# Kernel optimization log

Hardware: AMD Instinct MI355X
Metric: run time of the kernel (lower is better)

Reference implementation:

```python
import jax, jax.numpy as jnp
import numpy as np

N = 50000      # nodes
E = 800000     # edges (before self-loops)
D = 128        # hid_d
H = 8          # heads
C = D // H     # per-head channels
L = 3          # layers
SLOPE = 0.2    # GATv2 leaky_relu negative slope
EPS = 1e-5     # LayerNorm eps


def setup_inputs() -> dict:
    key = jax.random.key(0)
    ks = jax.random.split(key, 8)
    x = jax.random.normal(ks[0], (N, D), dtype=jnp.float32)
    ei = jax.random.randint(ks[1], (2, E), 0, N, dtype=jnp.int32)
    s = 1.0 / np.sqrt(D)
    Wl = jax.random.normal(ks[2], (L, D, D), dtype=jnp.float32) * s   # source transform per layer
    Wr = jax.random.normal(ks[3], (L, D, D), dtype=jnp.float32) * s   # target transform per layer
    att = jax.random.normal(ks[4], (L, H, C), dtype=jnp.float32) * (1.0 / np.sqrt(C))
    bias = jnp.zeros((L, D), dtype=jnp.float32)
    gamma = jnp.ones((L, D), dtype=jnp.float32)
    beta = jnp.zeros((L, D), dtype=jnp.float32)
    return {"x": x, "Wl": Wl, "Wr": Wr, "att": att, "bias": bias,
            "gamma": gamma, "beta": beta, "ei": ei}


def _layernorm(y, g, b):
    mu = jnp.mean(y, axis=-1, keepdims=True)
    var = jnp.mean(jnp.square(y - mu), axis=-1, keepdims=True)
    return (y - mu) * jax.lax.rsqrt(var + EPS) * g + b


def reference(x, Wl, Wr, att, bias, gamma, beta, ei):
    # append self-loops (PyG GATv2Conv default add_self_loops=True)
    loops = jnp.arange(N, dtype=ei.dtype)
    src = jnp.concatenate([ei[0], loops])  # [E+N]
    dst = jnp.concatenate([ei[1], loops])  # [E+N]
    h = x
    for l in range(L):
        xl = (h @ Wl[l]).reshape(N, H, C)   # source-side features
        xr = (h @ Wr[l]).reshape(N, H, C)   # target-side features
        feat = xl[src] + xr[dst]            # [E+N, H, C] per-edge gather
        logits = jnp.einsum('ehc,hc->eh', jax.nn.leaky_relu(feat, SLOPE), att[l])
        # segment softmax over incoming edges of each dst node
        m = jax.ops.segment_max(logits, dst, num_segments=N)
        ex = jnp.exp(logits - m[dst])
        denom = jax.ops.segment_sum(ex, dst, num_segments=N)
        alpha = ex / denom[dst]             # [E+N, H]
        msg = alpha[:, :, None] * xl[src]   # [E+N, H, C]
        out = jax.ops.segment_sum(msg, dst, num_segments=N).reshape(N, H * C) + bias[l]
        # wrapper: h = h + dropout(elu(norm(gat(h)))) ; dropout = identity (eval)
        h = h + jax.nn.elu(_layernorm(out, gamma[l], beta[l]))
    return h
```

## Files before the change

### kernel.cpp

```cpp
#include <hip/hip_runtime.h>
#include <hip/hip_fp16.h>
#include <math.h>

#define N_NODES 50000
#define N_EDGES 800000
#define D 128
#define L 3
#define SLOPE 0.2f
#define LN_EPS 1e-5f
#define ETOT (N_EDGES + N_NODES)
#define SCAN_BLOCKS ((N_NODES + 1023) / 1024)

typedef _Float16 half8 __attribute__((ext_vector_type(8)));
typedef float f32x4 __attribute__((ext_vector_type(4)));


__global__ void hist_kernel(const int* __restrict__ ei, int* __restrict__ counts) {
    int idx = blockIdx.x * blockDim.x + threadIdx.x;
    if (idx >= ETOT) return;
    int d = (idx < N_EDGES) ? ei[N_EDGES + idx] : (idx - N_EDGES);
    atomicAdd(&counts[d], 1);
}

__global__ __launch_bounds__(1024) void scan1_kernel(const int* __restrict__ counts,
                                                     int* __restrict__ offsets,
                                                     int* __restrict__ bsum) {
    __shared__ int wsum[16];
    int tid = threadIdx.x;
    int lane = tid & 63, w = tid >> 6;
    int i = blockIdx.x * 1024 + tid;
    int v = (i < N_NODES) ? counts[i] : 0;
    int sc = v;
    #pragma unroll
    for (int off = 1; off < 64; off <<= 1) {
        int u = __shfl_up(sc, off);
        if (lane >= off) sc += u;
    }
    if (lane == 63) wsum[w] = sc;
    __syncthreads();
    if (w == 0) {
        int t2 = (lane < 16) ? wsum[lane] : 0;
        #pragma unroll
        for (int off = 1; off < 16; off <<= 1) {
            int u = __shfl_up(t2, off);
            if (lane >= off) t2 += u;
        }
        if (lane < 16) wsum[lane] = t2;
    }
    __syncthreads();
    int wpref = (w == 0) ? 0 : wsum[w - 1];
    if (i < N_NODES) offsets[i] = wpref + sc - v;
    if (tid == 0) bsum[blockIdx.x] = wsum[15];
}

__global__ __launch_bounds__(64) void scan2_kernel(const int* __restrict__ bsum,
                                                   int* __restrict__ bpre) {
    int lane = threadIdx.x;
    int v = (lane < SCAN_BLOCKS) ? bsum[lane] : 0;
    int sc = v;
    #pragma unroll
    for (int off = 1; off < 64; off <<= 1) {
        int u = __shfl_up(sc, off);
        if (lane >= off) sc += u;
    }
    if (lane < SCAN_BLOCKS) bpre[lane] = sc - v;
}

__global__ __launch_bounds__(1024) void scan3_kernel(int* __restrict__ offsets,
                                                     const int* __restrict__ bpre) {
    int i = blockIdx.x * 1024 + threadIdx.x;
    if (i < N_NODES) offsets[i] += bpre[blockIdx.x];
    if (i == 0) offsets[N_NODES] = ETOT;
}

__global__ void scatter_kernel(const int* __restrict__ ei, const int* __restrict__ offsets,
                               int* __restrict__ cursor, int* __restrict__ sorted_src) {
    int idx = blockIdx.x * blockDim.x + threadIdx.x;
    if (idx >= ETOT) return;
    int s, d;
    if (idx < N_EDGES) { s = ei[idx]; d = ei[N_EDGES + idx]; }
    else               { s = d = idx - N_EDGES; }
    int pos = offsets[d] + atomicAdd(&cursor[d], 1);
    sorted_src[pos] = s;
}


__global__ __launch_bounds__(256) void wfrag_kernel(const float* __restrict__ Wl,
                                                    const float* __restrict__ Wr,
                                                    _Float16* __restrict__ Wfrag) {
    int u = blockIdx.x * 256 + threadIdx.x;
    if (u >= 3 * 4096) return;
    int lane = u & 63, nt = (u >> 6) & 7, kt = (u >> 9) & 3, y = (u >> 11) & 1, l = u >> 12;
    int r = lane & 15, q = lane >> 4;
    const float* W = (y ? Wr : Wl) + (size_t)l * D * D;
    half8 v;
    #pragma unroll
    for (int j = 0; j < 8; ++j)
        v[j] = (_Float16)W[(kt * 32 + q * 8 + j) * D + nt * 16 + r];
    *(half8*)&Wfrag[(size_t)u * 8] = v;
}


__global__ __launch_bounds__(256) void gemm_mfma_kernel(
        const float* __restrict__ h, const _Float16* __restrict__ WfragL,
        _Float16* __restrict__ xlh, _Float16* __restrict__ xrh) {
    __shared__ half8 Afrag[1024];
    int t = threadIdx.x;
    int row0 = blockIdx.x * 64;
    #pragma unroll
    for (int i = 0; i < 4; ++i) {
        int kt = t >> 6, q = (t >> 4) & 3, r = t & 15;
        int row = row0 + i * 16 + r;
        int kc = kt * 4 + q;
        float4 f0 = make_float4(0.f, 0.f, 0.f, 0.f), f1 = f0;
        if (row < N_NODES) {
            const float* p = &h[(size_t)row * D + kc * 8];
            f0 = *(const float4*)p;
            f1 = *(const float4*)(p + 4);
        }
        half8 v;
        v[0] = (_Float16)f0.x; v[1] = (_Float16)f0.y;
        v[2] = (_Float16)f0.z; v[3] = (_Float16)f0.w;
        v[4] = (_Float16)f1.x; v[5] = (_Float16)f1.y;
        v[6] = (_Float16)f1.z; v[7] = (_Float16)f1.w;
        Afrag[i * 256 + t] = v;
    }
    __syncthreads();
    const _Float16* Bf = WfragL + (size_t)blockIdx.y * 2048 * 8;
    int w = t >> 6, lane = t & 63;
    f32x4 acc[8];
    #pragma unroll
    for (int nt = 0; nt < 8; ++nt) acc[nt] = (f32x4){0.f, 0.f, 0.f, 0.f};
    #pragma unroll
    for (int kt = 0; kt < 4; ++kt) {
        half8 a = Afrag[(w * 4 + kt) * 64 + lane];
        #pragma unroll
        for (int nt = 0; nt < 8; ++nt) {
            half8 b = *(const half8*)&Bf[(size_t)((kt * 8 + nt) * 64 + lane) * 8];
            acc[nt] = __builtin_amdgcn_mfma_f32_16x16x32_f16(a, b, acc[nt], 0, 0, 0);
        }
    }
    _Float16* out = blockIdx.y ? xrh : xlh;
    int rq = lane >> 4, rc = lane & 15;
    int rbase = row0 + w * 16 + rq * 4;
    #pragma unroll
    for (int nt = 0; nt < 8; ++nt) {
        #pragma unroll
        for (int reg = 0; reg < 4; ++reg) {
            int row = rbase + reg;
            if (row < N_NODES)
                out[(size_t)row * D + nt * 16 + rc] = (_Float16)acc[nt][reg];
        }
    }
}


__device__ __forceinline__ float head_reduce8(float p) {
    int t;
    t = __builtin_amdgcn_update_dpp(0, __float_as_int(p), 0xB1, 0xF, 0xF, true);
    p += __int_as_float(t);
    t = __builtin_amdgcn_update_dpp(0, __float_as_int(p), 0x4E, 0xF, 0xF, true);
    p += __int_as_float(t);
    t = __builtin_amdgcn_update_dpp(0, __float_as_int(p), 0x141, 0xF, 0xF, true);
    p += __int_as_float(t);
    return p;
}

__device__ __forceinline__ float leaky(float f) { return fmaxf(f, SLOPE * f); }

__device__ __forceinline__ float edge_logit(float2 v, float2 xrv, float2 attv) {
    return fmaf(leaky(v.x + xrv.x), attv.x, leaky(v.y + xrv.y) * attv.y);
}

__global__ __launch_bounds__(256) void gat_node_kernel(
        const __half* __restrict__ xlh, const __half* __restrict__ xrh,
        const int* __restrict__ offsets, const int* __restrict__ sorted_src,
        const float* __restrict__ att_l, const float* __restrict__ bias_l,
        const float* __restrict__ gamma_l, const float* __restrict__ beta_l,
        const float* __restrict__ hin, float* __restrict__ hout) {
    int node = (blockIdx.x * blockDim.x + threadIdx.x) >> 6;
    if (node >= N_NODES) return;
    int lane = threadIdx.x & 63;
    unsigned laneoff = lane * 4u;
    float2 xrv  = __half22float2(((const __half2*)xrh)[(size_t)node * 64 + lane]);
    float2 attv = *(const float2*)&att_l[2 * lane];
    int beg = offsets[node], end = offsets[node + 1];
    float s = 0.f, accx = 0.f, accy = 0.f;
    const char* xlb = (const char*)xlh;
    for (int c0 = beg; c0 < end; c0 += 64) {
        int cnt = end - c0; if (cnt > 64) cnt = 64;
        int idx = sorted_src[c0 + (lane < cnt ? lane : cnt - 1)];
        unsigned off = (unsigned)idx << 8;
        int j = 0;
        for (; j + 8 <= cnt; j += 8) {
            unsigned o0 = __builtin_amdgcn_readlane(off, j)     + laneoff;
            unsigned o1 = __builtin_amdgcn_readlane(off, j + 1) + laneoff;
            unsigned o2 = __builtin_amdgcn_readlane(off, j + 2) + laneoff;
            unsigned o3 = __builtin_amdgcn_readlane(off, j + 3) + laneoff;
            unsigned o4 = __builtin_amdgcn_readlane(off, j + 4) + laneoff;
            unsigned o5 = __builtin_amdgcn_readlane(off, j + 5) + laneoff;
            unsigned o6 = __builtin_amdgcn_readlane(off, j + 6) + laneoff;
            unsigned o7 = __builtin_amdgcn_readlane(off, j + 7) + laneoff;
            float2 v0 = __half22float2(*(const __half2*)(xlb + o0));
            float2 v1 = __half22float2(*(const __half2*)(xlb + o1));
            float2 v2 = __half22float2(*(const __half2*)(xlb + o2));
            float2 v3 = __half22float2(*(const __half2*)(xlb + o3));
            float2 v4 = __half22float2(*(const __half2*)(xlb + o4));
            float2 v5 = __half22float2(*(const __half2*)(xlb + o5));
            float2 v6 = __half22float2(*(const __half2*)(xlb + o6));
            float2 v7 = __half22float2(*(const __half2*)(xlb + o7));
            float p0 = edge_logit(v0, xrv, attv);
            float p1 = edge_logit(v1, xrv, attv);
            float p2 = edge_logit(v2, xrv, attv);
            float p3 = edge_logit(v3, xrv, attv);
            float p4 = edge_logit(v4, xrv, attv);
            float p5 = edge_logit(v5, xrv, attv);
            float p6 = edge_logit(v6, xrv, attv);
            float p7 = edge_logit(v7, xrv, attv);
            p0 = head_reduce8(p0); p1 = head_reduce8(p1);
            p2 = head_reduce8(p2); p3 = head_reduce8(p3);
            p4 = head_reduce8(p4); p5 = head_reduce8(p5);
            p6 = head_reduce8(p6); p7 = head_reduce8(p7);
            float e0 = __expf(p0), e1 = __expf(p1);
            float e2 = __expf(p2), e3 = __expf(p3);
            float e4 = __expf(p4), e5 = __expf(p5);
            float e6 = __expf(p6), e7 = __expf(p7);
            s += ((e0 + e1) + (e2 + e3)) + ((e4 + e5) + (e6 + e7));
            accx = fmaf(e0, v0.x, accx); accy = fmaf(e0, v0.y, accy);
            accx = fmaf(e1, v1.x, accx); accy = fmaf(e1, v1.y, accy);
            accx = fmaf(e2, v2.x, accx); accy = fmaf(e2, v2.y, accy);
            accx = fmaf(e3, v3.x, accx); accy = fmaf(e3, v3.y, accy);
            accx = fmaf(e4, v4.x, accx); accy = fmaf(e4, v4.y, accy);
            accx = fmaf(e5, v5.x, accx); accy = fmaf(e5, v5.y, accy);
            accx = fmaf(e6, v6.x, accx); accy = fmaf(e6, v6.y, accy);
            accx = fmaf(e7, v7.x, accx); accy = fmaf(e7, v7.y, accy);
        }
        for (; j < cnt; ++j) {
            unsigned o0 = __builtin_amdgcn_readlane(off, j) + laneoff;
            float2 v0 = __half22float2(*(const __half2*)(xlb + o0));
            float p0 = edge_logit(v0, xrv, attv);
            p0 = head_reduce8(p0);
            float e0 = __expf(p0);
            s += e0;
            accx = fmaf(e0, v0.x, accx);
            accy = fmaf(e0, v0.y, accy);
        }
    }
    float inv = 1.f / s;
    float2 bia = *(const float2*)&bias_l[2 * lane];
    float o0 = accx * inv + bia.x;
    float o1 = accy * inv + bia.y;
    float sum = o0 + o1, sq = o0 * o0 + o1 * o1;
    #pragma unroll
    for (int msk = 1; msk < 64; msk <<= 1) {
        sum += __shfl_xor(sum, msk);
        sq  += __shfl_xor(sq, msk);
    }
    float mu   = sum * (1.f / 128.f);
    float var  = sq * (1.f / 128.f) - mu * mu;
    float rstd = rsqrtf(var + LN_EPS);
    float2 gam = *(const float2*)&gamma_l[2 * lane];
    float2 bet = *(const float2*)&beta_l[2 * lane];
    float y0 = (o0 - mu) * rstd * gam.x + bet.x;
    float y1 = (o1 - mu) * rstd * gam.y + bet.y;
    y0 = y0 > 0.f ? y0 : __expf(y0) - 1.f;
    y1 = y1 > 0.f ? y1 : __expf(y1) - 1.f;
    size_t di = (size_t)node * D + 2 * lane;
    float2 hv = *(const float2*)&hin[di];
    hv.x += y0; hv.y += y1;
    *(float2*)&hout[di] = hv;
}


extern "C" void kernel_launch(void* const* d_in, const int* in_sizes, int n_in,
                              void* d_out, int out_size, void* d_ws, size_t ws_size,
                              hipStream_t stream) {
    const float* x     = (const float*)d_in[0];
    const float* Wl    = (const float*)d_in[1];
    const float* Wr    = (const float*)d_in[2];
    const float* att   = (const float*)d_in[3];
    const float* bias  = (const float*)d_in[4];
    const float* gamma = (const float*)d_in[5];
    const float* beta  = (const float*)d_in[6];
    const int*   ei    = (const int*)d_in[7];
    float* h = (float*)d_out;

    char* ws = (char*)d_ws;
    _Float16* xlh = (_Float16*)ws;   ws += (size_t)N_NODES * D * sizeof(_Float16);
    _Float16* xrh = (_Float16*)ws;   ws += (size_t)N_NODES * D * sizeof(_Float16);
    _Float16* Wfrag = (_Float16*)ws; ws += (size_t)3 * 4096 * 8 * sizeof(_Float16);
    int* offsets = (int*)ws;         ws += (size_t)(N_NODES + 4) * sizeof(int);
    int* counts  = (int*)ws;         ws += (size_t)N_NODES * sizeof(int);
    int* bsum    = (int*)ws;         ws += 64 * sizeof(int);
    int* bpre    = (int*)ws;         ws += 64 * sizeof(int);
    int* sorted_src = (int*)ws;

    wfrag_kernel<<<48, 256, 0, stream>>>(Wl, Wr, Wfrag);
    hipMemsetAsync(counts, 0, (size_t)N_NODES * sizeof(int), stream);
    hist_kernel<<<(ETOT + 255) / 256, 256, 0, stream>>>(ei, counts);
    scan1_kernel<<<SCAN_BLOCKS, 1024, 0, stream>>>(counts, offsets, bsum);
    scan2_kernel<<<1, 64, 0, stream>>>(bsum, bpre);
    scan3_kernel<<<SCAN_BLOCKS, 1024, 0, stream>>>(offsets, bpre);
    hipMemsetAsync(counts, 0, (size_t)N_NODES * sizeof(int), stream);
    scatter_kernel<<<(ETOT + 255) / 256, 256, 0, stream>>>(ei, offsets, counts, sorted_src);

    dim3 ggrid((N_NODES + 63) / 64, 2);
    for (int l = 0; l < L; ++l) {
        const float* hin = (l == 0) ? x : h;
        gemm_mfma_kernel<<<ggrid, 256, 0, stream>>>(
            hin, Wfrag + (size_t)l * 4096 * 8, xlh, xrh);
        gat_node_kernel<<<(N_NODES * 64 + 255) / 256, 256, 0, stream>>>(
            (const __half*)xlh, (const __half*)xrh, offsets, sorted_src,
            att + (size_t)l * D, bias + (size_t)l * D,
            gamma + (size_t)l * D, beta + (size_t)l * D, hin, h);
    }
}
```

Measured before the change: 371.5 us.

## Record edge ranks, use 16-bit sorted indices, fuse xl/xr GEMM, fp16 dot-product logits

```diff
diff --git a/kernel.cpp b/kernel.cpp
--- a/kernel.cpp
+++ b/kernel.cpp
@@ -12,14 +12,16 @@
 #define SCAN_BLOCKS ((N_NODES + 1023) / 1024)
 
 typedef _Float16 half8 __attribute__((ext_vector_type(8)));
+typedef _Float16 h2v  __attribute__((ext_vector_type(2)));
 typedef float f32x4 __attribute__((ext_vector_type(4)));
 
 
-__global__ void hist_kernel(const int* __restrict__ ei, int* __restrict__ counts) {
+__global__ void rank_hist_kernel(const int* __restrict__ ei, int* __restrict__ counts,
+                                 int* __restrict__ rank) {
     int idx = blockIdx.x * blockDim.x + threadIdx.x;
     if (idx >= ETOT) return;
     int d = (idx < N_EDGES) ? ei[N_EDGES + idx] : (idx - N_EDGES);
-    atomicAdd(&counts[d], 1);
+    rank[idx] = atomicAdd(&counts[d], 1);
 }
 
 __global__ __launch_bounds__(1024) void scan1_kernel(const int* __restrict__ counts,
@@ -74,14 +76,14 @@
 }
 
 __global__ void scatter_kernel(const int* __restrict__ ei, const int* __restrict__ offsets,
-                               int* __restrict__ cursor, int* __restrict__ sorted_src) {
+                               const int* __restrict__ rank,
+                               unsigned short* __restrict__ sorted16) {
     int idx = blockIdx.x * blockDim.x + threadIdx.x;
     if (idx >= ETOT) return;
     int s, d;
     if (idx < N_EDGES) { s = ei[idx]; d = ei[N_EDGES + idx]; }
     else               { s = d = idx - N_EDGES; }
-    int pos = offsets[d] + atomicAdd(&cursor[d], 1);
-    sorted_src[pos] = s;
+    sorted16[offsets[d] + rank[idx]] = (unsigned short)s;
 }
 
 
@@ -107,49 +109,56 @@
     __shared__ half8 Afrag[1024];
     int t = threadIdx.x;
     int row0 = blockIdx.x * 64;
-    #pragma unroll
-    for (int i = 0; i < 4; ++i) {
+    {
         int kt = t >> 6, q = (t >> 4) & 3, r = t & 15;
-        int row = row0 + i * 16 + r;
         int kc = kt * 4 + q;
-        float4 f0 = make_float4(0.f, 0.f, 0.f, 0.f), f1 = f0;
-        if (row < N_NODES) {
-            const float* p = &h[(size_t)row * D + kc * 8];
-            f0 = *(const float4*)p;
-            f1 = *(const float4*)(p + 4);
-        }
-        half8 v;
-        v[0] = (_Float16)f0.x; v[1] = (_Float16)f0.y;
-        v[2] = (_Float16)f0.z; v[3] = (_Float16)f0.w;
-        v[4] = (_Float16)f1.x; v[5] = (_Float16)f1.y;
-        v[6] = (_Float16)f1.z; v[7] = (_Float16)f1.w;
-        Afrag[i * 256 + t] = v;
+        #pragma unroll
+        for (int i = 0; i < 4; ++i) {
+            int row = row0 + i * 16 + r;
+            float4 f0 = make_float4(0.f, 0.f, 0.f, 0.f), f1 = f0;
+            if (row < N_NODES) {
+                const float* p = &h[(size_t)row * D + kc * 8];
+                f0 = *(const float4*)p;
+                f1 = *(const float4*)(p + 4);
+            }
+            half8 v;
+            v[0] = (_Float16)f0.x; v[1] = (_Float16)f0.y;
+            v[2] = (_Float16)f0.z; v[3] = (_Float16)f0.w;
+            v[4] = (_Float16)f1.x; v[5] = (_Float16)f1.y;
+            v[6] = (_Float16)f1.z; v[7] = (_Float16)f1.w;
+            Afrag[i * 256 + t] = v;
+        }
     }
     __syncthreads();
-    const _Float16* Bf = WfragL + (size_t)blockIdx.y * 2048 * 8;
     int w = t >> 6, lane = t & 63;
-    f32x4 acc[8];
-    #pragma unroll
-    for (int nt = 0; nt < 8; ++nt) acc[nt] = (f32x4){0.f, 0.f, 0.f, 0.f};
+    f32x4 acc[16];
+    #pragma unroll
+    for (int i = 0; i < 16; ++i) acc[i] = (f32x4){0.f, 0.f, 0.f, 0.f};
     #pragma unroll
     for (int kt = 0; kt < 4; ++kt) {
         half8 a = Afrag[(w * 4 + kt) * 64 + lane];
         #pragma unroll
-        for (int nt = 0; nt < 8; ++nt) {
-            half8 b = *(const half8*)&Bf[(size_t)((kt * 8 + nt) * 64 + lane) * 8];
-            acc[nt] = __builtin_amdgcn_mfma_f32_16x16x32_f16(a, b, acc[nt], 0, 0, 0);
-        }
-    }
-    _Float16* out = blockIdx.y ? xrh : xlh;
+        for (int y = 0; y < 2; ++y) {
+            #pragma unroll
+            for (int nt = 0; nt < 8; ++nt) {
+                half8 b = *(const half8*)&WfragL[(size_t)(((y * 4 + kt) * 8 + nt) * 64 + lane) * 8];
+                acc[y * 8 + nt] = __builtin_amdgcn_mfma_f32_16x16x32_f16(a, b, acc[y * 8 + nt], 0, 0, 0);
+            }
+        }
+    }
     int rq = lane >> 4, rc = lane & 15;
     int rbase = row0 + w * 16 + rq * 4;
     #pragma unroll
-    for (int nt = 0; nt < 8; ++nt) {
+    for (int y = 0; y < 2; ++y) {
+        _Float16* out = y ? xrh : xlh;
         #pragma unroll
-        for (int reg = 0; reg < 4; ++reg) {
-            int row = rbase + reg;
-            if (row < N_NODES)
-                out[(size_t)row * D + nt * 16 + rc] = (_Float16)acc[nt][reg];
+        for (int nt = 0; nt < 8; ++nt) {
+            #pragma unroll
+            for (int reg = 0; reg < 4; ++reg) {
+                int row = rbase + reg;
+                if (row < N_NODES)
+                    out[(size_t)row * D + nt * 16 + rc] = (_Float16)acc[y * 8 + nt][reg];
+            }
         }
     }
 }
@@ -166,15 +175,19 @@
     return p;
 }
 
-__device__ __forceinline__ float leaky(float f) { return fmaxf(f, SLOPE * f); }
-
-__device__ __forceinline__ float edge_logit(float2 v, float2 xrv, float2 attv) {
-    return fmaf(leaky(v.x + xrv.x), attv.x, leaky(v.y + xrv.y) * attv.y);
+__device__ __forceinline__ float logit2(h2v v, h2v xrv2, h2v att2, h2v slope2) {
+    h2v f  = v + xrv2;
+    h2v lf = __builtin_elementwise_max(f, f * slope2);
+    return __builtin_amdgcn_fdot2(lf, att2, 0.f, false);
+}
+
+__device__ __forceinline__ float2 h2f(h2v v) {
+    return make_float2((float)v[0], (float)v[1]);
 }
 
 __global__ __launch_bounds__(256) void gat_node_kernel(
-        const __half* __restrict__ xlh, const __half* __restrict__ xrh,
-        const int* __restrict__ offsets, const int* __restrict__ sorted_src,
+        const _Float16* __restrict__ xlh, const _Float16* __restrict__ xrh,
+        const int* __restrict__ offsets, const unsigned short* __restrict__ sorted16,
         const float* __restrict__ att_l, const float* __restrict__ bias_l,
         const float* __restrict__ gamma_l, const float* __restrict__ beta_l,
         const float* __restrict__ hin, float* __restrict__ hout) {
@@ -182,15 +195,21 @@
     if (node >= N_NODES) return;
     int lane = threadIdx.x & 63;
     unsigned laneoff = lane * 4u;
-    float2 xrv  = __half22float2(((const __half2*)xrh)[(size_t)node * 64 + lane]);
-    float2 attv = *(const float2*)&att_l[2 * lane];
+    h2v xrv2 = ((const h2v*)xrh)[(size_t)node * 64 + lane];
+    float2 attf = *(const float2*)&att_l[2 * lane];
+    h2v att2;
+    att2[0] = (_Float16)(attf.x * 1.44269504f);
+    att2[1] = (_Float16)(attf.y * 1.44269504f);
+    h2v slope2;
+    slope2[0] = (_Float16)SLOPE;
+    slope2[1] = (_Float16)SLOPE;
     int beg = offsets[node], end = offsets[node + 1];
     float s = 0.f, accx = 0.f, accy = 0.f;
     const char* xlb = (const char*)xlh;
     for (int c0 = beg; c0 < end; c0 += 64) {
         int cnt = end - c0; if (cnt > 64) cnt = 64;
-        int idx = sorted_src[c0 + (lane < cnt ? lane : cnt - 1)];
-        unsigned off = (unsigned)idx << 8;
+        unsigned idx = sorted16[c0 + (lane < cnt ? lane : cnt - 1)];
+        unsigned off = idx << 8;
         int j = 0;
         for (; j + 8 <= cnt; j += 8) {
             unsigned o0 = __builtin_amdgcn_readlane(off, j)     + laneoff;
@@ -201,49 +220,54 @@
             unsigned o5 = __builtin_amdgcn_readlane(off, j + 5) + laneoff;
             unsigned o6 = __builtin_amdgcn_readlane(off, j + 6) + laneoff;
             unsigned o7 = __builtin_amdgcn_readlane(off, j + 7) + laneoff;
-            float2 v0 = __half22float2(*(const __half2*)(xlb + o0));
-            float2 v1 = __half22float2(*(const __half2*)(xlb + o1));
-            float2 v2 = __half22float2(*(const __half2*)(xlb + o2));
-            float2 v3 = __half22float2(*(const __half2*)(xlb + o3));
-            float2 v4 = __half22float2(*(const __half2*)(xlb + o4));
-            float2 v5 = __half22float2(*(const __half2*)(xlb + o5));
-            float2 v6 = __half22float2(*(const __half2*)(xlb + o6));
-            float2 v7 = __half22float2(*(const __half2*)(xlb + o7));
-            float p0 = edge_logit(v0, xrv, attv);
-            float p1 = edge_logit(v1, xrv, attv);
-            float p2 = edge_logit(v2, xrv, attv);
-            float p3 = edge_logit(v3, xrv, attv);
-            float p4 = edge_logit(v4, xrv, attv);
-            float p5 = edge_logit(v5, xrv, attv);
-            float p6 = edge_logit(v6, xrv, attv);
-            float p7 = edge_logit(v7, xrv, attv);
+            h2v v0 = *(const h2v*)(xlb + o0);
+            h2v v1 = *(const h2v*)(xlb + o1);
+            h2v v2 = *(const h2v*)(xlb + o2);
+            h2v v3 = *(const h2v*)(xlb + o3);
+            h2v v4 = *(const h2v*)(xlb + o4);
+            h2v v5 = *(const h2v*)(xlb + o5);
+            h2v v6 = *(const h2v*)(xlb + o6);
+            h2v v7 = *(const h2v*)(xlb + o7);
+            float p0 = logit2(v0, xrv2, att2, slope2);
+            float p1 = logit2(v1, xrv2, att2, slope2);
+            float p2 = logit2(v2, xrv2, att2, slope2);
+            float p3 = logit2(v3, xrv2, att2, slope2);
+            float p4 = logit2(v4, xrv2, att2, slope2);
+            float p5 = logit2(v5, xrv2, att2, slope2);
+            float p6 = logit2(v6, xrv2, att2, slope2);
+            float p7 = logit2(v7, xrv2, att2, slope2);
             p0 = head_reduce8(p0); p1 = head_reduce8(p1);
             p2 = head_reduce8(p2); p3 = head_reduce8(p3);
             p4 = head_reduce8(p4); p5 = head_reduce8(p5);
             p6 = head_reduce8(p6); p7 = head_reduce8(p7);
-            float e0 = __expf(p0), e1 = __expf(p1);
-            float e2 = __expf(p2), e3 = __expf(p3);
-            float e4 = __expf(p4), e5 = __expf(p5);
-            float e6 = __expf(p6), e7 = __expf(p7);
+            float e0 = __builtin_amdgcn_exp2f(p0), e1 = __builtin_amdgcn_exp2f(p1);
+            float e2 = __builtin_amdgcn_exp2f(p2), e3 = __builtin_amdgcn_exp2f(p3);
+            float e4 = __builtin_amdgcn_exp2f(p4), e5 = __builtin_amdgcn_exp2f(p5);
+            float e6 = __builtin_amdgcn_exp2f(p6), e7 = __builtin_amdgcn_exp2f(p7);
             s += ((e0 + e1) + (e2 + e3)) + ((e4 + e5) + (e6 + e7));
-            accx = fmaf(e0, v0.x, accx); accy = fmaf(e0, v0.y, accy);
-            accx = fmaf(e1, v1.x, accx); accy = fmaf(e1, v1.y, accy);
-            accx = fmaf(e2, v2.x, accx); accy = fmaf(e2, v2.y, accy);
-            accx = fmaf(e3, v3.x, accx); accy = fmaf(e3, v3.y, accy);
-            accx = fmaf(e4, v4.x, accx); accy = fmaf(e4, v4.y, accy);
-            accx = fmaf(e5, v5.x, accx); accy = fmaf(e5, v5.y, accy);
-            accx = fmaf(e6, v6.x, accx); accy = fmaf(e6, v6.y, accy);
-            accx = fmaf(e7, v7.x, accx); accy = fmaf(e7, v7.y, accy);
+            float2 f0 = h2f(v0), f1 = h2f(v1);
+            float2 f2 = h2f(v2), f3 = h2f(v3);
+            float2 f4 = h2f(v4), f5 = h2f(v5);
+            float2 f6 = h2f(v6), f7 = h2f(v7);
+            accx = fmaf(e0, f0.x, accx); accy = fmaf(e0, f0.y, accy);
+            accx = fmaf(e1, f1.x, accx); accy = fmaf(e1, f1.y, accy);
+            accx = fmaf(e2, f2.x, accx); accy = fmaf(e2, f2.y, accy);
+            accx = fmaf(e3, f3.x, accx); accy = fmaf(e3, f3.y, accy);
+            accx = fmaf(e4, f4.x, accx); accy = fmaf(e4, f4.y, accy);
+            accx = fmaf(e5, f5.x, accx); accy = fmaf(e5, f5.y, accy);
+            accx = fmaf(e6, f6.x, accx); accy = fmaf(e6, f6.y, accy);
+            accx = fmaf(e7, f7.x, accx); accy = fmaf(e7, f7.y, accy);
         }
         for (; j < cnt; ++j) {
             unsigned o0 = __builtin_amdgcn_readlane(off, j) + laneoff;
-            float2 v0 = __half22float2(*(const __half2*)(xlb + o0));
-            float p0 = edge_logit(v0, xrv, attv);
+            h2v v0 = *(const h2v*)(xlb + o0);
+            float p0 = logit2(v0, xrv2, att2, slope2);
             p0 = head_reduce8(p0);
-            float e0 = __expf(p0);
+            float e0 = __builtin_amdgcn_exp2f(p0);
             s += e0;
-            accx = fmaf(e0, v0.x, accx);
-            accy = fmaf(e0, v0.y, accy);
+            float2 f0 = h2f(v0);
+            accx = fmaf(e0, f0.x, accx);
+            accy = fmaf(e0, f0.y, accy);
         }
     }
     float inv = 1.f / s;
@@ -293,24 +317,23 @@
     int* counts  = (int*)ws;         ws += (size_t)N_NODES * sizeof(int);
     int* bsum    = (int*)ws;         ws += 64 * sizeof(int);
     int* bpre    = (int*)ws;         ws += 64 * sizeof(int);
-    int* sorted_src = (int*)ws;
+    int* rank    = (int*)ws;         ws += (size_t)ETOT * sizeof(int);
+    unsigned short* sorted16 = (unsigned short*)ws;
 
     wfrag_kernel<<<48, 256, 0, stream>>>(Wl, Wr, Wfrag);
-    hipMemsetAsync(counts, 0, (size_t)N_NODES * sizeof(int), stream);
-    hist_kernel<<<(ETOT + 255) / 256, 256, 0, stream>>>(ei, counts);
+    (void)hipMemsetAsync(counts, 0, (size_t)N_NODES * sizeof(int), stream);
+    rank_hist_kernel<<<(ETOT + 255) / 256, 256, 0, stream>>>(ei, counts, rank);
     scan1_kernel<<<SCAN_BLOCKS, 1024, 0, stream>>>(counts, offsets, bsum);
     scan2_kernel<<<1, 64, 0, stream>>>(bsum, bpre);
     scan3_kernel<<<SCAN_BLOCKS, 1024, 0, stream>>>(offsets, bpre);
-    hipMemsetAsync(counts, 0, (size_t)N_NODES * sizeof(int), stream);
-    scatter_kernel<<<(ETOT + 255) / 256, 256, 0, stream>>>(ei, offsets, counts, sorted_src);
-
-    dim3 ggrid((N_NODES + 63) / 64, 2);
+    scatter_kernel<<<(ETOT + 255) / 256, 256, 0, stream>>>(ei, offsets, rank, sorted16);
+
     for (int l = 0; l < L; ++l) {
         const float* hin = (l == 0) ? x : h;
-        gemm_mfma_kernel<<<ggrid, 256, 0, stream>>>(
+        gemm_mfma_kernel<<<(N_NODES + 63) / 64, 256, 0, stream>>>(
             hin, Wfrag + (size_t)l * 4096 * 8, xlh, xrh);
         gat_node_kernel<<<(N_NODES * 64 + 255) / 256, 256, 0, stream>>>(
-            (const __half*)xlh, (const __half*)xrh, offsets, sorted_src,
+            xlh, xrh, offsets, sorted16,
             att + (size_t)l * D, bias + (size_t)l * D,
             gamma + (size_t)l * D, beta + (size_t)l * D, hin, h);
     }
```

After: 340.2 us. -8.4%, faster.
